# Kernel tuning notes

Hardware: AMD Instinct MI355X
Metric: run time of the kernel (lower is better)

The kernel has to match this reference:

```python
import jax, jax.numpy as jnp
import numpy as np

N = 100000   # num_nodes
E = 600000   # num_edges (before self loops)
H = 128      # hidden_size
R = 16       # lora_rank
SCALING = 32.0 / 16  # lora_alpha / lora_rank
LN_EPS = 1e-5


def setup_inputs() -> dict:
    key = jax.random.key(0)
    ks = jax.random.split(key, 12)
    s = 0.02
    return {
        "hidden_states": jax.random.normal(ks[0], (N, H), dtype=jnp.float32),
        "edge_index": jax.random.randint(ks[1], (2, E), 0, N, dtype=jnp.int64),
        # message_transform (LoRALinear): base W/b + lora A/B
        "msg_W": jax.random.normal(ks[2], (H, H), dtype=jnp.float32) * s,
        "msg_b": jax.random.normal(ks[3], (H,), dtype=jnp.float32) * s,
        "msg_A": jax.random.normal(ks[4], (R, H), dtype=jnp.float32) * s,
        "msg_B": jax.random.normal(ks[5], (H, R), dtype=jnp.float32) * s,
        # gate_transform (LoRALinear)
        "gate_W": jax.random.normal(ks[6], (H, H), dtype=jnp.float32) * s,
        "gate_b": jax.random.normal(ks[7], (H,), dtype=jnp.float32) * s,
        "gate_A": jax.random.normal(ks[8], (R, H), dtype=jnp.float32) * s,
        "gate_B": jax.random.normal(ks[9], (H, R), dtype=jnp.float32) * s,
        # LayerNorm params
        "ln_gamma": jnp.ones((H,), dtype=jnp.float32),
        "ln_beta": jnp.zeros((H,), dtype=jnp.float32),
    }


def _lora_linear(x, W, b, A, B):
    # base_layer(x) + scaling * lora_B(lora_A(x)); dropout is identity at eval
    return x @ W.T + b + SCALING * ((x @ A.T) @ B.T)


def _message_passing(x, edge_index):
    n = x.shape[0]
    loops = jnp.arange(n, dtype=edge_index.dtype)
    row = jnp.concatenate([edge_index[0], loops])  # sources j
    col = jnp.concatenate([edge_index[1], loops])  # targets i
    # symmetric-ish norm: deg from targets (PyG degree(col))
    deg = jax.ops.segment_sum(jnp.ones_like(col, dtype=x.dtype), col, num_segments=n)
    dinv = jnp.where(deg > 0, deg ** -0.5, 0.0)
    norm = dinv[row] * dinv[col]                   # [E+N]
    msgs = norm[:, None] * x[row]                  # edge-gathered messages
    summed = jax.ops.segment_sum(msgs, col, num_segments=n)
    # aggr='mean': divide by per-target edge count (== deg, includes self loop)
    return summed / jnp.maximum(deg, 1.0)[:, None]


def reference(hidden_states, edge_index, msg_W, msg_b, msg_A, msg_B,
              gate_W, gate_b, gate_A, gate_B, ln_gamma, ln_beta):
    message_out = _message_passing(hidden_states, edge_index)
    message_transformed = _lora_linear(message_out, msg_W, msg_b, msg_A, msg_B)
    gate = jax.nn.sigmoid(_lora_linear(hidden_states, gate_W, gate_b, gate_A, gate_B))
    x = hidden_states + gate * message_transformed
    mu = jnp.mean(x, axis=-1, keepdims=True)
    var = jnp.mean(jnp.square(x - mu), axis=-1, keepdims=True)
    return (x - mu) / jnp.sqrt(var + LN_EPS) * ln_gamma + ln_beta
```

## Files before the change

### kernel.cpp

```cpp
#include <hip/hip_runtime.h>
#include <math.h>

#define H 128
#define RANK 16
#define SCALING 2.0f
#define LN_EPS 1e-5f
#define PAD 48

typedef short bf16x8 __attribute__((ext_vector_type(8)));
typedef float f32x4 __attribute__((ext_vector_type(4)));

__device__ __forceinline__ unsigned short f2bf(float f) {
    unsigned int u = __float_as_uint(f);
    u += 0x7fffu + ((u >> 16) & 1u);
    return (unsigned short)(u >> 16);
}
__device__ __forceinline__ unsigned int pk2(float a, float b) {
    return (unsigned int)f2bf(a) | ((unsigned int)f2bf(b) << 16);
}
__device__ __forceinline__ float bflo(unsigned int u) {
    return __uint_as_float(u << 16);
}
__device__ __forceinline__ float bfhi(unsigned int u) {
    return __uint_as_float(u & 0xffff0000u);
}

__global__ __launch_bounds__(256) void k_init(
    const int* __restrict__ ei, int E,
    int* __restrict__ deg, int* __restrict__ adj,
    const float4* __restrict__ x4, int total16, unsigned int* __restrict__ xb,
    const float* __restrict__ msg_W, const float* __restrict__ msg_A,
    const float* __restrict__ msg_B,
    const float* __restrict__ gate_W, const float* __restrict__ gate_A,
    const float* __restrict__ gate_B,
    unsigned short* __restrict__ Wmz, unsigned short* __restrict__ Wgz,
    int BA, int BB) {
    int b = blockIdx.x;
    int t = threadIdx.x;
    if (b < BA) {
        int q = b * 256 + t;
        int e0 = q * 8;
        if ((E & 7) == 0) {
            if (e0 < E) {
                const int4* colv = (const int4*)(ei + E);
                const int4* srcv = (const int4*)ei;
                int4 c0 = colv[q * 2], c1 = colv[q * 2 + 1];
                int4 s0 = srcv[q * 2], s1 = srcv[q * 2 + 1];
                int cc[8] = {c0.x, c0.y, c0.z, c0.w, c1.x, c1.y, c1.z, c1.w};
                int ss[8] = {s0.x, s0.y, s0.z, s0.w, s1.x, s1.y, s1.z, s1.w};
                int pos[8];
                #pragma unroll
                for (int j = 0; j < 8; ++j) pos[j] = atomicAdd(&deg[cc[j]], 1);
                #pragma unroll
                for (int j = 0; j < 8; ++j)
                    if (pos[j] < PAD) adj[cc[j] * PAD + pos[j]] = ss[j];
            }
        } else {
            #pragma unroll
            for (int j = 0; j < 8; ++j) {
                int e = e0 + j;
                if (e < E) {
                    int c = ei[E + e];
                    int pos = atomicAdd(&deg[c], 1);
                    if (pos < PAD) adj[c * PAD + pos] = ei[e];
                }
            }
        }
    } else if (b < BA + BB) {
        int idx = (b - BA) * 256 + t;
        if (idx < total16) {
            float4 a = x4[idx * 4 + 0];
            float4 bq = x4[idx * 4 + 1];
            float4 cq = x4[idx * 4 + 2];
            float4 dq = x4[idx * 4 + 3];
            uint4 o0, o1;
            o0.x = pk2(a.x, a.y);   o0.y = pk2(a.z, a.w);
            o0.z = pk2(bq.x, bq.y); o0.w = pk2(bq.z, bq.w);
            o1.x = pk2(cq.x, cq.y); o1.y = pk2(cq.z, cq.w);
            o1.z = pk2(dq.x, dq.y); o1.w = pk2(dq.z, dq.w);
            uint4* xb4 = (uint4*)xb;
            xb4[idx * 2 + 0] = o0;
            xb4[idx * 2 + 1] = o1;
        }
    } else {
        int bb = b - BA - BB;
        int which = bb >> 6;
        int idx = (bb & 63) * 256 + t;
        const float* W = which ? gate_W : msg_W;
        const float* A = which ? gate_A : msg_A;
        const float* Bm = which ? gate_B : msg_B;
        unsigned short* Wz = which ? Wgz : Wmz;
        int h = idx & (H - 1);
        int k = idx >> 7;
        float s = 0.f;
        #pragma unroll
        for (int r = 0; r < RANK; ++r) s = fmaf(A[r * H + k], Bm[h * RANK + r], s);
        float v = W[h * H + k] + SCALING * s;
        int kt = k >> 5, kk = k & 31, qd = kk >> 3, j = kk & 7;
        int nt = h >> 4, nl = h & 15;
        int lane = qd * 16 + nl;
        Wz[(((kt * 8 + nt) * 64 + lane) * 8) + j] = f2bf(v);
    }
}

__global__ __launch_bounds__(256) void k_gather(
    const unsigned int* __restrict__ xb, const int* __restrict__ adj,
    const int* __restrict__ deg, int N, unsigned int* __restrict__ msgb) {
    int wave = (blockIdx.x * 256 + threadIdx.x) >> 6;
    int lane = threadIdx.x & 63;
    if (wave >= N) return;
    int i = __builtin_amdgcn_readfirstlane(wave);
    int dg = __builtin_amdgcn_readfirstlane(deg[i]);
    float dif = (float)(dg + 1);
    float di = rsqrtf(dif);
    unsigned int su = xb[(size_t)i * 64 + lane];
    float ax[8], ay[8];
    ax[0] = bflo(su) * di; ay[0] = bfhi(su) * di;
    #pragma unroll
    for (int j = 1; j < 8; ++j) { ax[j] = 0.f; ay[j] = 0.f; }
    int cnt = dg < PAD ? dg : PAD;
    int s0 = i * PAD, s1 = s0 + cnt;
    int last = s1 - 1;
    for (int e = s0; e < s1; e += 8) {
        int is[8]; float ws[8]; unsigned int us[8];
        #pragma unroll
        for (int j = 0; j < 8; ++j) {
            int ee = e + j;
            is[j] = __builtin_amdgcn_readfirstlane(adj[ee < s1 ? ee : last]);
        }
        #pragma unroll
        for (int j = 0; j < 8; ++j) {
            float w = rsqrtf((float)(deg[is[j]] + 1));
            ws[j] = (e + j < s1) ? w : 0.f;
        }
        #pragma unroll
        for (int j = 0; j < 8; ++j) us[j] = xb[(size_t)is[j] * 64 + lane];
        #pragma unroll
        for (int j = 0; j < 8; ++j) {
            ax[j] = fmaf(ws[j], bflo(us[j]), ax[j]);
            ay[j] = fmaf(ws[j], bfhi(us[j]), ay[j]);
        }
    }
    float sc = di / dif;
    float rx = (((ax[0] + ax[1]) + (ax[2] + ax[3])) + ((ax[4] + ax[5]) + (ax[6] + ax[7]))) * sc;
    float ry = (((ay[0] + ay[1]) + (ay[2] + ay[3])) + ((ay[4] + ay[5]) + (ay[6] + ay[7]))) * sc;
    msgb[(size_t)i * 64 + lane] = (unsigned int)f2bf(rx) | ((unsigned int)f2bf(ry) << 16);
}

__global__ __launch_bounds__(256) void k_fused(
    const unsigned int* __restrict__ xb, const unsigned int* __restrict__ msgb,
    const unsigned short* __restrict__ Wmz, const unsigned short* __restrict__ Wgz,
    const float* __restrict__ msg_b, const float* __restrict__ gate_b,
    const float* __restrict__ gamma, const float* __restrict__ beta,
    float* __restrict__ out, int N) {
    __shared__ unsigned int hLds[64 * 64];
    __shared__ float oLds[4][8 * 132];
    int t = threadIdx.x;
    int wid = t >> 6, lane = t & 63;
    int m0 = (blockIdx.x * 4 + wid) * 16;
    if (m0 >= N) return;

    char* rowbase = (char*)(hLds + wid * 16 * 64);

    #pragma unroll
    for (int r16 = 0; r16 < 16; ++r16) {
        int rr = m0 + r16; if (rr >= N) rr = N - 1;
        unsigned int v = xb[(size_t)rr * 64 + lane];
        int wbyte = ((r16 * 64 + lane) << 2) ^ ((r16 & 7) << 4);
        *(unsigned int*)(rowbase + wbyte) = v;
    }

    int quad = lane >> 4;
    int nl = lane & 15;

    int arow = m0 + nl; if (arow >= N) arow = N - 1;
    const bf16x8* mb8 = (const bf16x8*)msgb + (size_t)arow * 16;

    f32x4 accg[8], accm[8];
    #pragma unroll
    for (int nt = 0; nt < 8; ++nt) {
        accg[nt] = (f32x4)(0.f);
        accm[nt] = (f32x4)(0.f);
    }

    #pragma unroll
    for (int kt = 0; kt < 4; ++kt) {
        int abyte = (nl * 256 + kt * 64 + quad * 16) ^ ((nl & 7) << 4);
        bf16x8 ah = *(const bf16x8*)(rowbase + abyte);
        bf16x8 am = mb8[kt * 4 + quad];
        const bf16x8* bg8 = (const bf16x8*)(Wgz + (size_t)kt * 4096);
        const bf16x8* bm8 = (const bf16x8*)(Wmz + (size_t)kt * 4096);
        #pragma unroll
        for (int nt = 0; nt < 8; ++nt) {
            bf16x8 bg = bg8[nt * 64 + lane];
            bf16x8 bm = bm8[nt * 64 + lane];
            accg[nt] = __builtin_amdgcn_mfma_f32_16x16x32_bf16(ah, bg, accg[nt], 0, 0, 0);
            accm[nt] = __builtin_amdgcn_mfma_f32_16x16x32_bf16(am, bm, accm[nt], 0, 0, 0);
        }
    }

    float gb[8], mb[8], gm[8], bt[8];
    #pragma unroll
    for (int nt = 0; nt < 8; ++nt) {
        int col = nt * 16 + nl;
        gb[nt] = gate_b[col]; mb[nt] = msg_b[col];
        gm[nt] = gamma[col];  bt[nt] = beta[col];
    }

    float* owave = oLds[wid];
    #pragma unroll
    for (int c = 0; c < 2; ++c) {
        #pragma unroll
        for (int rc = 0; rc < 2; ++rc) {
            int r = c * 2 + rc;
            int row = quad * 4 + r;
            float xr[8]; float s = 0.f, ss = 0.f;
            #pragma unroll
            for (int nt = 0; nt < 8; ++nt) {
                int col = nt * 16 + nl;
                int hbyte = (row * 256 + col * 2) ^ ((row & 7) << 4);
                unsigned short hu = *(const unsigned short*)(rowbase + hbyte);
                float hv = __uint_as_float((unsigned int)hu << 16);
                float g = 1.f / (1.f + __expf(-(accg[nt][r] + gb[nt])));
                float m = accm[nt][r] + mb[nt];
                float v = fmaf(g, m, hv);
                xr[nt] = v; s += v; ss = fmaf(v, v, ss);
            }
            #pragma unroll
            for (int msk = 1; msk < 16; msk <<= 1) {
                s += __shfl_xor(s, msk);
                ss += __shfl_xor(ss, msk);
            }
            float mu = s * (1.f / 128.f);
            float var = ss * (1.f / 128.f) - mu * mu;
            float rstd = rsqrtf(var + LN_EPS);
            float* orow_l = owave + (quad * 2 + rc) * 132;
            #pragma unroll
            for (int nt = 0; nt < 8; ++nt)
                orow_l[nt * 16 + nl] = (xr[nt] - mu) * rstd * gm[nt] + bt[nt];
        }
        #pragma unroll
        for (int k = 0; k < 4; ++k) {
            int f = k * 64 + lane;
            int slot = f >> 5, c4 = f & 31;
            int node = m0 + (slot >> 1) * 4 + c * 2 + (slot & 1);
            float4 v = *(float4*)&owave[slot * 132 + c4 * 4];
            if (node < N) *(float4*)(out + (size_t)node * H + c4 * 4) = v;
        }
    }
}

extern "C" void kernel_launch(void* const* d_in, const int* in_sizes, int n_in,
                              void* d_out, int out_size, void* d_ws, size_t ws_size,
                              hipStream_t stream) {
    const float* hidden = (const float*)d_in[0];
    const int*   ei     = (const int*)d_in[1];
    const float* msg_W  = (const float*)d_in[2];
    const float* msg_b  = (const float*)d_in[3];
    const float* msg_A  = (const float*)d_in[4];
    const float* msg_B  = (const float*)d_in[5];
    const float* gate_W = (const float*)d_in[6];
    const float* gate_b = (const float*)d_in[7];
    const float* gate_A = (const float*)d_in[8];
    const float* gate_B = (const float*)d_in[9];
    const float* gamma  = (const float*)d_in[10];
    const float* beta   = (const float*)d_in[11];
    float* out = (float*)d_out;

    int N = in_sizes[0] / H;
    int E = in_sizes[1] / 2;

    char* p = (char*)d_ws;
    unsigned short* Wmz = (unsigned short*)p;  p += (size_t)H * H * sizeof(unsigned short);
    unsigned short* Wgz = (unsigned short*)p;  p += (size_t)H * H * sizeof(unsigned short);
    unsigned int* xb   = (unsigned int*)p;     p += (size_t)N * 64 * sizeof(unsigned int);
    unsigned int* msgb = (unsigned int*)p;     p += (size_t)N * 64 * sizeof(unsigned int);
    int* deg = (int*)p;                        p += (size_t)N * sizeof(int);

    int* adj = (int*)d_out;

    hipMemsetAsync(deg, 0, (size_t)N * sizeof(int), stream);

    int BA = (E + 2047) / 2048;
    int total16 = (N * H) >> 4;
    int BB = (total16 + 255) / 256;

    k_init<<<BA + BB + 128, 256, 0, stream>>>(
        ei, E, deg, adj, (const float4*)hidden, total16, xb,
        msg_W, msg_A, msg_B, gate_W, gate_A, gate_B, Wmz, Wgz, BA, BB);

    k_gather<<<((size_t)N * 64 + 255) / 256, 256, 0, stream>>>(
        xb, adj, deg, N, msgb);

    int waves = (N + 15) / 16;
    k_fused<<<(waves + 3) / 4, 256, 0, stream>>>(
        xb, msgb, Wmz, Wgz, msg_b, gate_b, gamma, beta, out, N);
}
```

Before: 231.0 us.

## Make gather kernel persistent with software prefetch of next node's data

Converts the one-wave-per-node gather kernel into a persistent grid-stride kernel with a fixed grid, where each wave prefetches the next node's degree, self features and first eight neighbor indices while processing the current node. The first eight-edge batch uses those prefetched indices, and the accumulators shrink from eight to four per lane. The goal is to hide the dependent latency of the deg-to-adj-to-xb load chain and cut launch/wave startup overhead. The cost is fewer waves in flight, which may reduce memory-level parallelism, plus extra registers for the prefetch state.

```diff
diff --git a/kernel.cpp b/kernel.cpp
--- a/kernel.cpp
+++ b/kernel.cpp
@@ -6,6 +6,7 @@
 #define SCALING 2.0f
 #define LN_EPS 1e-5f
 #define PAD 48
+#define GBLK 2048
 
 typedef short bf16x8 __attribute__((ext_vector_type(8)));
 typedef float f32x4 __attribute__((ext_vector_type(4)));
@@ -106,45 +107,91 @@
 __global__ __launch_bounds__(256) void k_gather(
     const unsigned int* __restrict__ xb, const int* __restrict__ adj,
     const int* __restrict__ deg, int N, unsigned int* __restrict__ msgb) {
-    int wave = (blockIdx.x * 256 + threadIdx.x) >> 6;
     int lane = threadIdx.x & 63;
-    if (wave >= N) return;
-    int i = __builtin_amdgcn_readfirstlane(wave);
-    int dg = __builtin_amdgcn_readfirstlane(deg[i]);
-    float dif = (float)(dg + 1);
-    float di = rsqrtf(dif);
-    unsigned int su = xb[(size_t)i * 64 + lane];
-    float ax[8], ay[8];
-    ax[0] = bflo(su) * di; ay[0] = bfhi(su) * di;
-    #pragma unroll
-    for (int j = 1; j < 8; ++j) { ax[j] = 0.f; ay[j] = 0.f; }
-    int cnt = dg < PAD ? dg : PAD;
-    int s0 = i * PAD, s1 = s0 + cnt;
-    int last = s1 - 1;
-    for (int e = s0; e < s1; e += 8) {
-        int is[8]; float ws[8]; unsigned int us[8];
-        #pragma unroll
-        for (int j = 0; j < 8; ++j) {
-            int ee = e + j;
-            is[j] = __builtin_amdgcn_readfirstlane(adj[ee < s1 ? ee : last]);
-        }
-        #pragma unroll
-        for (int j = 0; j < 8; ++j) {
-            float w = rsqrtf((float)(deg[is[j]] + 1));
-            ws[j] = (e + j < s1) ? w : 0.f;
-        }
-        #pragma unroll
-        for (int j = 0; j < 8; ++j) us[j] = xb[(size_t)is[j] * 64 + lane];
-        #pragma unroll
-        for (int j = 0; j < 8; ++j) {
-            ax[j] = fmaf(ws[j], bflo(us[j]), ax[j]);
-            ay[j] = fmaf(ws[j], bfhi(us[j]), ay[j]);
-        }
-    }
-    float sc = di / dif;
-    float rx = (((ax[0] + ax[1]) + (ax[2] + ax[3])) + ((ax[4] + ax[5]) + (ax[6] + ax[7]))) * sc;
-    float ry = (((ay[0] + ay[1]) + (ay[2] + ay[3])) + ((ay[4] + ay[5]) + (ay[6] + ay[7]))) * sc;
-    msgb[(size_t)i * 64 + lane] = (unsigned int)f2bf(rx) | ((unsigned int)f2bf(ry) << 16);
+    int gw = (blockIdx.x * 256 + threadIdx.x) >> 6;
+    int NW = (gridDim.x * 256) >> 6;
+    int cur = gw;
+    if (cur >= N) return;
+
+    int pi = __builtin_amdgcn_readfirstlane(cur);
+    int pdg = deg[pi];
+    unsigned int psu = xb[(size_t)pi * 64 + lane];
+    int pis[8];
+    #pragma unroll
+    for (int j = 0; j < 8; ++j) pis[j] = adj[pi * PAD + j];
+
+    while (true) {
+        int i = pi;
+        int dg = __builtin_amdgcn_readfirstlane(pdg);
+        unsigned int su = psu;
+        int is0[8];
+        #pragma unroll
+        for (int j = 0; j < 8; ++j) is0[j] = __builtin_amdgcn_readfirstlane(pis[j]);
+
+        int nxt = cur + NW;
+        int more = (nxt < N);
+        int pn = more ? nxt : i;
+        pi = __builtin_amdgcn_readfirstlane(pn);
+        pdg = deg[pi];
+        psu = xb[(size_t)pi * 64 + lane];
+        #pragma unroll
+        for (int j = 0; j < 8; ++j) pis[j] = adj[pi * PAD + j];
+
+        float dif = (float)(dg + 1);
+        float di = rsqrtf(dif);
+        float ax[4], ay[4];
+        ax[0] = bflo(su) * di; ay[0] = bfhi(su) * di;
+        #pragma unroll
+        for (int j = 1; j < 4; ++j) { ax[j] = 0.f; ay[j] = 0.f; }
+        int cnt = dg < PAD ? dg : PAD;
+
+        {
+            float ws[8]; unsigned int us[8]; int idx[8];
+            #pragma unroll
+            for (int j = 0; j < 8; ++j)
+                idx[j] = __builtin_amdgcn_readfirstlane(j < cnt ? is0[j] : i);
+            #pragma unroll
+            for (int j = 0; j < 8; ++j) {
+                float w = rsqrtf((float)(deg[idx[j]] + 1));
+                ws[j] = (j < cnt) ? w : 0.f;
+            }
+            #pragma unroll
+            for (int j = 0; j < 8; ++j) us[j] = xb[(size_t)idx[j] * 64 + lane];
+            #pragma unroll
+            for (int j = 0; j < 8; ++j) {
+                ax[j & 3] = fmaf(ws[j], bflo(us[j]), ax[j & 3]);
+                ay[j & 3] = fmaf(ws[j], bfhi(us[j]), ay[j & 3]);
+            }
+        }
+        for (int e = 8; e < cnt; e += 8) {
+            int is[8]; float ws[8]; unsigned int us[8];
+            #pragma unroll
+            for (int j = 0; j < 8; ++j) {
+                int ee = e + j;
+                is[j] = __builtin_amdgcn_readfirstlane(ee < cnt ? adj[i * PAD + ee] : i);
+            }
+            #pragma unroll
+            for (int j = 0; j < 8; ++j) {
+                float w = rsqrtf((float)(deg[is[j]] + 1));
+                ws[j] = (e + j < cnt) ? w : 0.f;
+            }
+            #pragma unroll
+            for (int j = 0; j < 8; ++j) us[j] = xb[(size_t)is[j] * 64 + lane];
+            #pragma unroll
+            for (int j = 0; j < 8; ++j) {
+                ax[j & 3] = fmaf(ws[j], bflo(us[j]), ax[j & 3]);
+                ay[j & 3] = fmaf(ws[j], bfhi(us[j]), ay[j & 3]);
+            }
+        }
+
+        float sc = di / dif;
+        float rx = ((ax[0] + ax[1]) + (ax[2] + ax[3])) * sc;
+        float ry = ((ay[0] + ay[1]) + (ay[2] + ay[3])) * sc;
+        msgb[(size_t)i * 64 + lane] = pk2(rx, ry);
+
+        if (!more) break;
+        cur = nxt;
+    }
 }
 
 __global__ __launch_bounds__(256) void k_fused(
@@ -289,7 +336,7 @@
         ei, E, deg, adj, (const float4*)hidden, total16, xb,
         msg_W, msg_A, msg_B, gate_W, gate_A, gate_B, Wmz, Wgz, BA, BB);
 
-    k_gather<<<((size_t)N * 64 + 255) / 256, 256, 0, stream>>>(
+    k_gather<<<GBLK, 256, 0, stream>>>(
         xb, adj, deg, N, msgb);
 
     int waves = (N + 15) / 16;
```

New measurement: 224.5 us. 1.03x faster.
